# Performance work log

Measured on AMD Instinct MI355X. Metric: run time of the kernel, lower is better.

Reference implementation:

```python
import jax, jax.numpy as jnp
import numpy as np

WIN = 11      # window_size in pytorch_msssim
SIGMA = 1.5   # gaussian sigma in create_window
LEVELS = 5


def _gauss_window(channels, dtype):
    # 1D gaussian -> normalized 2D window, replicated per channel for depthwise conv
    x = jnp.arange(WIN, dtype=dtype) - WIN // 2
    g = jnp.exp(-(x * x) / (2.0 * SIGMA * SIGMA))
    g = g / jnp.sum(g)
    w2 = jnp.outer(g, g)  # [11,11]
    return jnp.broadcast_to(w2[None, None], (channels, 1, WIN, WIN))


def _dwconv(x, w):
    # depthwise valid conv, NCHW (matches F.conv2d(..., padding=0, groups=channel))
    return jax.lax.conv_general_dilated(
        x, w, window_strides=(1, 1), padding='VALID',
        dimension_numbers=('NCHW', 'OIHW', 'NCHW'),
        feature_group_count=x.shape[1])


def _ssim_cs(p, t, w):
    # pytorch_msssim.ssim with full=True, val_range L=1 (inputs in [0,1])
    C1 = 0.01 ** 2
    C2 = 0.03 ** 2
    mu1 = _dwconv(p, w)
    mu2 = _dwconv(t, w)
    mu1_sq = mu1 * mu1
    mu2_sq = mu2 * mu2
    mu1_mu2 = mu1 * mu2
    sigma1_sq = _dwconv(p * p, w) - mu1_sq
    sigma2_sq = _dwconv(t * t, w) - mu2_sq
    sigma12 = _dwconv(p * t, w) - mu1_mu2
    v1 = 2.0 * sigma12 + C2
    v2 = sigma1_sq + sigma2_sq + C2
    # per-category means (axis 1 = the 10 categories, batched as channels)
    cs = jnp.mean(v1 / v2, axis=(0, 2, 3))                                   # [C]
    sim = jnp.mean(((2.0 * mu1_mu2 + C1) * v1) / ((mu1_sq + mu2_sq + C1) * v2),
                   axis=(0, 2, 3))                                           # [C]
    return sim, cs


def _avg_pool2(x):
    n, c, h, w = x.shape
    return x.reshape(n, c, h // 2, 2, w // 2, 2).mean(axis=(3, 5))


def setup_inputs() -> dict:
    key = jax.random.key(0)
    k1, k2 = jax.random.split(key)
    y_pred = jax.random.uniform(k1, (10, 1024, 1024), dtype=jnp.float32)
    y_true = jax.random.uniform(k2, (10, 1024, 1024), dtype=jnp.float32)
    return {"y_pred": y_pred, "y_true": y_true}


def reference(y_pred, y_true):
    # MSSLoss.forward: loss = sum over 10 categories of msssim(pred[c], true[c]);
    # return 1 - mean(loss)  (loss is a scalar, so mean is identity).
    # All 10 per-category msssim calls are batched as channels of one depthwise conv.
    dtype = y_pred.dtype
    weights = jnp.array([0.0448, 0.2856, 0.3001, 0.2363, 0.1333], dtype=dtype)
    p = y_pred[None]  # [1,10,H,W]
    t = y_true[None]
    w = _gauss_window(p.shape[1], dtype)
    sims, css = [], []
    for _ in range(LEVELS):
        s, c = _ssim_cs(p, t, w)
        sims.append(s)
        css.append(c)
        p = _avg_pool2(p)
        t = _avg_pool2(t)
    mssim = jnp.stack(sims)  # [5, 10]
    mcs = jnp.stack(css)     # [5, 10]
    pow1 = mcs ** weights[:, None]
    pow2 = mssim ** weights[:, None]
    # Po-Hsun-Su pytorch_msssim: output = torch.prod(pow1[:-1] * pow2[-1])
    per_cat = jnp.prod(pow1[:-1] * pow2[-1][None, :], axis=0)  # [10]
    return 1.0 - jnp.sum(per_cat)
```

## Files before the change

kernel.cpp:

```cpp
#include <hip/hip_runtime.h>
#include <cstddef>

#define WIN 11
#define HALO 10
#define NCH 10

typedef float v4f __attribute__((ext_vector_type(4)));

constexpr float Gc[WIN] = {
    0.00102838f, 0.00759876f, 0.03600077f, 0.10936069f, 0.21300554f,
    0.26601173f, 0.21300554f, 0.10936069f, 0.03600077f, 0.00759876f,
    0.00102838f};

constexpr int HPITCH = 33;
constexpr int RS = 76;
constexpr int RSZ = RS * HPITCH;

struct Ptrs {
    const float* p[5];
    const float* t[5];
};

__global__ __launch_bounds__(256) void pool_all(
    const float* __restrict__ P0, const float* __restrict__ T0,
    float* __restrict__ p1, float* __restrict__ t1,
    float* __restrict__ p2, float* __restrict__ t2,
    float* __restrict__ p3, float* __restrict__ t3,
    float* __restrict__ p4, float* __restrict__ t4,
    float* __restrict__ acc) {
    __shared__ float sp2[256], st2[256], sp3[64], st3[64];
    const int tid = threadIdx.x;
    if (blockIdx.x == 0 && tid < 128) acc[tid] = 0.f;

    const int b = blockIdx.x;
    const int bx = b & 15, by = (b >> 4) & 15, ch = b >> 8;
    const int tx = tid & 15, ty = tid >> 4;

    const size_t rbase =
        ((size_t)ch * 1024 + by * 64 + ty * 4) * 1024 + bx * 64 + tx * 4;
    float4 pr[4], tr[4];
#pragma unroll
    for (int r2 = 0; r2 < 4; ++r2) {
        pr[r2] = *(const float4*)(P0 + rbase + (size_t)r2 * 1024);
        tr[r2] = *(const float4*)(T0 + rbase + (size_t)r2 * 1024);
    }
    float p1a = 0.25f * ((pr[0].x + pr[0].y) + (pr[1].x + pr[1].y));
    float p1b = 0.25f * ((pr[0].z + pr[0].w) + (pr[1].z + pr[1].w));
    float p1c = 0.25f * ((pr[2].x + pr[2].y) + (pr[3].x + pr[3].y));
    float p1d = 0.25f * ((pr[2].z + pr[2].w) + (pr[3].z + pr[3].w));
    float t1a = 0.25f * ((tr[0].x + tr[0].y) + (tr[1].x + tr[1].y));
    float t1b = 0.25f * ((tr[0].z + tr[0].w) + (tr[1].z + tr[1].w));
    float t1c = 0.25f * ((tr[2].x + tr[2].y) + (tr[3].x + tr[3].y));
    float t1d = 0.25f * ((tr[2].z + tr[2].w) + (tr[3].z + tr[3].w));
    size_t o1 = ((size_t)ch * 512 + by * 32 + ty * 2) * 512 + bx * 32 + tx * 2;
    *(float2*)(p1 + o1) = make_float2(p1a, p1b);
    *(float2*)(p1 + o1 + 512) = make_float2(p1c, p1d);
    *(float2*)(t1 + o1) = make_float2(t1a, t1b);
    *(float2*)(t1 + o1 + 512) = make_float2(t1c, t1d);
    float p2v = 0.25f * ((p1a + p1b) + (p1c + p1d));
    float t2v = 0.25f * ((t1a + t1b) + (t1c + t1d));
    size_t o2 = ((size_t)ch * 256 + by * 16 + ty) * 256 + bx * 16 + tx;
    p2[o2] = p2v;
    t2[o2] = t2v;
    sp2[tid] = p2v;
    st2[tid] = t2v;
    __syncthreads();
    if (tid < 64) {
        int x3 = tid & 7, y3 = tid >> 3;
        int i0 = (2 * y3) * 16 + 2 * x3;
        float p3v = 0.25f * ((sp2[i0] + sp2[i0 + 1]) + (sp2[i0 + 16] + sp2[i0 + 17]));
        float t3v = 0.25f * ((st2[i0] + st2[i0 + 1]) + (st2[i0 + 16] + st2[i0 + 17]));
        size_t o3 = ((size_t)ch * 128 + by * 8 + y3) * 128 + bx * 8 + x3;
        p3[o3] = p3v;
        t3[o3] = t3v;
        sp3[tid] = p3v;
        st3[tid] = t3v;
    }
    __syncthreads();
    if (tid < 16) {
        int x4 = tid & 3, y4 = tid >> 2;
        int i0 = (2 * y4) * 8 + 2 * x4;
        float p4v = 0.25f * ((sp3[i0] + sp3[i0 + 1]) + (sp3[i0 + 8] + sp3[i0 + 9]));
        float t4v = 0.25f * ((st3[i0] + st3[i0 + 1]) + (st3[i0 + 8] + st3[i0 + 9]));
        size_t o4 = ((size_t)ch * 64 + by * 4 + y4) * 64 + bx * 4 + x4;
        p4[o4] = p4v;
        t4[o4] = t4v;
    }
}

__global__ __launch_bounds__(256) void ssim_strip(Ptrs ptrs,
                                                  float* __restrict__ acc) {
    __shared__ v4f hq[RSZ];
    __shared__ float red[8];

    const int bxi = blockIdx.x;
    int lvl, base;
    if (bxi < 128)      { lvl = 0; base = 0; }
    else if (bxi < 160) { lvl = 1; base = 128; }
    else if (bxi < 168) { lvl = 2; base = 160; }
    else if (bxi < 172) { lvl = 3; base = 168; }
    else                { lvl = 4; base = 172; }
    const int local = bxi - base;
    const int H = 1024 >> lvl;
    const int Wout = H - HALO;
    const int ncol = 32 >> lvl;
    const int cs = local & (ncol - 1);
    const int rsi = local >> (5 - lvl);
    const int X0 = cs * 32;
    const int strip_y0 = rsi * 256;
    const int strip_rows = min(256, Wout - strip_y0);
    const int rows_needed = strip_rows + HALO;
    const int nIter = (strip_rows + 31) >> 5;

    const int c = blockIdx.y;
    const float* Pc = ptrs.p[lvl] + (size_t)c * H * H;
    const float* Tc = ptrs.t[lvl] + (size_t)c * H * H;
    const int tid = threadIdx.x;
    const int r6 = tid / 6;
    const int seg = tid - r6 * 6;
    const int x0s = seg * 6;
    const int gxb = X0 + x0s;

    auto load_row = [&](int gy, float2 lp[8], float2 lt[8]) {
        const float* Pr = Pc + (size_t)gy * H + gxb;
        const float* Tr = Tc + (size_t)gy * H + gxb;
        if (gxb + 16 <= H) {
#pragma unroll
            for (int j = 0; j < 8; ++j) {
                lp[j] = *(const float2*)(Pr + 2 * j);
                lt[j] = *(const float2*)(Tr + 2 * j);
            }
        } else {
#pragma unroll
            for (int j = 0; j < 8; ++j) {
                float2 a = make_float2(0.f, 0.f), b = make_float2(0.f, 0.f);
                if (gxb + 2 * j < H)     { a.x = Pr[2 * j];     b.x = Tr[2 * j]; }
                if (gxb + 2 * j + 1 < H) { a.y = Pr[2 * j + 1]; b.y = Tr[2 * j + 1]; }
                lp[j] = a;
                lt[j] = b;
            }
        }
    };

    auto conv_store = [&](int rr, const float2 lp[8], const float2 lt[8]) {
        v4f aq[6] = {};
#pragma unroll
        for (int xi = 0; xi < 16; ++xi) {
            float pv = (xi & 1) ? lp[xi >> 1].y : lp[xi >> 1].x;
            float tv = (xi & 1) ? lt[xi >> 1].y : lt[xi >> 1].x;
            float pp = pv * pv, tt = tv * tv;
            v4f xq = (v4f){pv, tv, pp + tt, pv * tv};
#pragma unroll
            for (int o = 0; o < 6; ++o) {
                int k = xi - o;
                if (k >= 0 && k <= 10) {
                    aq[o] = aq[o] + Gc[k] * xq;
                }
            }
        }
        const int sb = rr * HPITCH;
#pragma unroll
        for (int o = 0; o < 6; ++o) {
            int x = x0s + o;
            if (x < 32) hq[sb + x] = aq[o];
        }
    };

    if (tid < 252) {
        float2 lp[8], lt[8];
        load_row(strip_y0 + r6, lp, lt);
        conv_store(r6, lp, lt);
    }
    __syncthreads();

    float cs_sum = 0.f, sim_sum = 0.f;
    const int txl = tid & 31;
    const int g4 = (tid >> 5) * 4;
    int rrm = r6 + 42;
    if (rrm >= RS) rrm -= RS;
    int y0m = 0;
    for (int i = 0; i < nIter; ++i) {
        float2 lp[8], lt[8];
        const int hrel = 42 + 32 * i + r6;
        const bool doS1 = (tid < 192) && (i + 1 < nIter) && (hrel < rows_needed);
        if (doS1) load_row(strip_y0 + hrel, lp, lt);

        {
            int sl = y0m + g4;
            if (sl >= RS) sl -= RS;
            v4f a[4] = {};
#pragma unroll
            for (int yr = 0; yr < 14; ++yr) {
                v4f vq = hq[sl * HPITCH + txl];
#pragma unroll
                for (int o = 0; o < 4; ++o) {
                    int k = yr - o;
                    if (k >= 0 && k <= 10) {
                        a[o] = a[o] + Gc[k] * vq;
                    }
                }
                ++sl;
                if (sl >= RS) sl = 0;
            }
            const float C1c = 1.0e-4f, C2c = 9.0e-4f;
            const bool colok = (X0 + txl) < Wout;
#pragma unroll
            for (int o = 0; o < 4; ++o) {
                if (colok && (32 * i + g4 + o) < strip_rows) {
                    float mu1 = a[o].x, mu2 = a[o].y;
                    float mu1s = mu1 * mu1, mu2s = mu2 * mu2, mu12 = mu1 * mu2;
                    float v2 = a[o].z - mu1s - mu2s + C2c;
                    float v1 = 2.f * (a[o].w - mu12) + C2c;
                    float den2 = mu1s + mu2s + C1c;
                    float num2 = 2.f * mu12 + C1c;
                    float inv = 1.f / (v2 * den2);
                    cs_sum = fmaf(v1 * den2, inv, cs_sum);
                    sim_sum = fmaf(num2 * v1, inv, sim_sum);
                }
            }
        }

        if (doS1) conv_store(rrm, lp, lt);
        rrm += 32;
        if (rrm >= RS) rrm -= RS;
        y0m += 32;
        if (y0m >= RS) y0m -= RS;
        __syncthreads();
    }

#pragma unroll
    for (int off = 32; off > 0; off >>= 1) {
        cs_sum += __shfl_down(cs_sum, off, 64);
        sim_sum += __shfl_down(sim_sum, off, 64);
    }
    int wave = tid >> 6;
    if ((tid & 63) == 0) {
        red[wave * 2 + 0] = sim_sum;
        red[wave * 2 + 1] = cs_sum;
    }
    __syncthreads();
    if (tid == 0) {
        float s = red[0] + red[2] + red[4] + red[6];
        float cc = red[1] + red[3] + red[5] + red[7];
        atomicAdd(&acc[(lvl * NCH + c) * 2 + 0], s);
        atomicAdd(&acc[(lvl * NCH + c) * 2 + 1], cc);
    }
}

__global__ void finalize_k(const float* __restrict__ acc, float* __restrict__ out) {
    if (threadIdx.x != 0) return;
    const double w[5] = {0.0448, 0.2856, 0.3001, 0.2363, 0.1333};
    const double counts[5] = {1014.0 * 1014.0, 502.0 * 502.0, 246.0 * 246.0,
                              118.0 * 118.0, 54.0 * 54.0};
    double total = 0.0;
    for (int c = 0; c < NCH; ++c) {
        double pc = 1.0;
        for (int l = 0; l < 4; ++l) {
            double mcs = (double)acc[(l * NCH + c) * 2 + 1] / counts[l];
            pc *= pow(mcs, w[l]);
        }
        double ms4 = (double)acc[(4 * NCH + c) * 2 + 0] / counts[4];
        double p2 = pow(ms4, w[4]);
        pc *= (p2 * p2) * (p2 * p2);
        total += pc;
    }
    *out = (float)(1.0 - total);
}

extern "C" void kernel_launch(void* const* d_in, const int* in_sizes, int n_in,
                              void* d_out, int out_size, void* d_ws, size_t ws_size,
                              hipStream_t stream) {
    const float* P0 = (const float*)d_in[0];
    const float* T0 = (const float*)d_in[1];
    float* out = (float*)d_out;
    float* acc = (float*)d_ws;

    const size_t n1 = (size_t)NCH * 512 * 512;
    const size_t n2 = (size_t)NCH * 256 * 256;
    const size_t n3 = (size_t)NCH * 128 * 128;
    const size_t n4 = (size_t)NCH * 64 * 64;
    float* p1 = acc + 128;
    float* t1 = p1 + n1;
    float* p2 = t1 + n1;
    float* t2 = p2 + n2;
    float* p3 = t2 + n2;
    float* t3 = p3 + n3;
    float* p4 = t3 + n3;
    float* t4 = p4 + n4;

    pool_all<<<2560, 256, 0, stream>>>(P0, T0, p1, t1, p2, t2, p3, t3, p4, t4, acc);

    Ptrs ptrs;
    ptrs.p[0] = P0; ptrs.t[0] = T0;
    ptrs.p[1] = p1; ptrs.t[1] = t1;
    ptrs.p[2] = p2; ptrs.t[2] = t2;
    ptrs.p[3] = p3; ptrs.t[3] = t3;
    ptrs.p[4] = p4; ptrs.t[4] = t4;

    ssim_strip<<<dim3(174, NCH, 1), 256, 0, stream>>>(ptrs, acc);

    finalize_k<<<1, 64, 0, stream>>>(acc, out);
}
```

Baseline: 209.7 us.

## Split block into producer and consumer waves for horizontal and vertical conv

The block is split into producer threads (upper half), which register-prefetch the next rows and write horizontal conv results into the shared ring buffer, and consumer threads (lower half), which run the vertical conv plus SSIM math. Each producer now computes 8 outputs from 18 inputs, and each consumer computes 8 output rows from 18 slots, replacing the old 6-wide and 4-row tiles to cut redundant halo work. The goal is to overlap global loads with compute and improve reuse. In exchange only half the threads do the vertical and SSIM math, and register pressure rises, which may lower occupancy.

```diff
diff --git a/kernel.cpp b/kernel.cpp
--- a/kernel.cpp
+++ b/kernel.cpp
@@ -116,23 +116,19 @@
     const float* Pc = ptrs.p[lvl] + (size_t)c * H * H;
     const float* Tc = ptrs.t[lvl] + (size_t)c * H * H;
     const int tid = threadIdx.x;
-    const int r6 = tid / 6;
-    const int seg = tid - r6 * 6;
-    const int x0s = seg * 6;
-    const int gxb = X0 + x0s;
-
-    auto load_row = [&](int gy, float2 lp[8], float2 lt[8]) {
+
+    auto load_row18 = [&](int gy, int gxb, float2 lp[9], float2 lt[9]) {
         const float* Pr = Pc + (size_t)gy * H + gxb;
         const float* Tr = Tc + (size_t)gy * H + gxb;
-        if (gxb + 16 <= H) {
-#pragma unroll
-            for (int j = 0; j < 8; ++j) {
+        if (gxb + 18 <= H) {
+#pragma unroll
+            for (int j = 0; j < 9; ++j) {
                 lp[j] = *(const float2*)(Pr + 2 * j);
                 lt[j] = *(const float2*)(Tr + 2 * j);
             }
         } else {
 #pragma unroll
-            for (int j = 0; j < 8; ++j) {
+            for (int j = 0; j < 9; ++j) {
                 float2 a = make_float2(0.f, 0.f), b = make_float2(0.f, 0.f);
                 if (gxb + 2 * j < H)     { a.x = Pr[2 * j];     b.x = Tr[2 * j]; }
                 if (gxb + 2 * j + 1 < H) { a.y = Pr[2 * j + 1]; b.y = Tr[2 * j + 1]; }
@@ -142,71 +138,79 @@
         }
     };
 
-    auto conv_store = [&](int rr, const float2 lp[8], const float2 lt[8]) {
-        v4f aq[6] = {};
-#pragma unroll
-        for (int xi = 0; xi < 16; ++xi) {
+    auto conv_store8 = [&](int rr, int x0, const float2 lp[9], const float2 lt[9]) {
+        v4f aq[8] = {};
+#pragma unroll
+        for (int xi = 0; xi < 18; ++xi) {
             float pv = (xi & 1) ? lp[xi >> 1].y : lp[xi >> 1].x;
             float tv = (xi & 1) ? lt[xi >> 1].y : lt[xi >> 1].x;
-            float pp = pv * pv, tt = tv * tv;
-            v4f xq = (v4f){pv, tv, pp + tt, pv * tv};
-#pragma unroll
-            for (int o = 0; o < 6; ++o) {
+            v4f xq = (v4f){pv, tv, pv * pv + tv * tv, pv * tv};
+#pragma unroll
+            for (int o = 0; o < 8; ++o) {
                 int k = xi - o;
-                if (k >= 0 && k <= 10) {
-                    aq[o] = aq[o] + Gc[k] * xq;
-                }
-            }
-        }
-        const int sb = rr * HPITCH;
-#pragma unroll
-        for (int o = 0; o < 6; ++o) {
-            int x = x0s + o;
-            if (x < 32) hq[sb + x] = aq[o];
-        }
+                if (k >= 0 && k <= 10) aq[o] = aq[o] + Gc[k] * xq;
+            }
+        }
+        const int sb = rr * HPITCH + x0;
+#pragma unroll
+        for (int o = 0; o < 8; ++o) hq[sb + o] = aq[o];
     };
 
-    if (tid < 252) {
-        float2 lp[8], lt[8];
-        load_row(strip_y0 + r6, lp, lt);
-        conv_store(r6, lp, lt);
+    {
+        const int r = tid >> 2, seg = tid & 3;
+        if (r < 42) {
+            float2 lp[9], lt[9];
+            load_row18(strip_y0 + r, X0 + 8 * seg, lp, lt);
+            conv_store8(r, 8 * seg, lp, lt);
+        }
+    }
+
+    const bool isProd = (tid >= 128);
+    const int pr = tid & 31;
+    const int pseg = (tid >> 5) & 3;
+    float2 plp[9], plt[9];
+    int prRow = 42 + pr;
+    int prSlot = prRow;
+    bool pHave = false;
+    if (isProd && prRow < rows_needed && nIter > 1) {
+        load_row18(strip_y0 + prRow, X0 + 8 * pseg, plp, plt);
+        pHave = true;
     }
     __syncthreads();
 
     float cs_sum = 0.f, sim_sum = 0.f;
     const int txl = tid & 31;
-    const int g4 = (tid >> 5) * 4;
-    int rrm = r6 + 42;
-    if (rrm >= RS) rrm -= RS;
+    const int g = (tid >> 5) & 3;
     int y0m = 0;
     for (int i = 0; i < nIter; ++i) {
-        float2 lp[8], lt[8];
-        const int hrel = 42 + 32 * i + r6;
-        const bool doS1 = (tid < 192) && (i + 1 < nIter) && (hrel < rows_needed);
-        if (doS1) load_row(strip_y0 + hrel, lp, lt);
-
-        {
-            int sl = y0m + g4;
+        if (isProd) {
+            if (pHave) conv_store8(prSlot, 8 * pseg, plp, plt);
+            prSlot += 32;
+            if (prSlot >= RS) prSlot -= RS;
+            prRow += 32;
+            pHave = (prRow < rows_needed) && (i + 2 < nIter + 1) && (i + 1 < nIter);
+            if (pHave) load_row18(strip_y0 + prRow, X0 + 8 * pseg, plp, plt);
+        } else {
+            int sl = y0m + 8 * g;
             if (sl >= RS) sl -= RS;
-            v4f a[4] = {};
-#pragma unroll
-            for (int yr = 0; yr < 14; ++yr) {
+            v4f a[8] = {};
+#pragma unroll
+            for (int yr = 0; yr < 18; ++yr) {
                 v4f vq = hq[sl * HPITCH + txl];
 #pragma unroll
-                for (int o = 0; o < 4; ++o) {
+                for (int o = 0; o < 8; ++o) {
                     int k = yr - o;
-                    if (k >= 0 && k <= 10) {
-                        a[o] = a[o] + Gc[k] * vq;
-                    }
+                    if (k >= 0 && k <= 10) a[o] = a[o] + Gc[k] * vq;
                 }
                 ++sl;
                 if (sl >= RS) sl = 0;
             }
             const float C1c = 1.0e-4f, C2c = 9.0e-4f;
             const bool colok = (X0 + txl) < Wout;
-#pragma unroll
-            for (int o = 0; o < 4; ++o) {
-                if (colok && (32 * i + g4 + o) < strip_rows) {
+            const int orow0 = 32 * i + 8 * g;
+#pragma unroll
+            for (int o = 0; o < 8; ++o) {
+                if (colok && (orow0 + o) < strip_rows) {
                     float mu1 = a[o].x, mu2 = a[o].y;
                     float mu1s = mu1 * mu1, mu2s = mu2 * mu2, mu12 = mu1 * mu2;
                     float v2 = a[o].z - mu1s - mu2s + C2c;
@@ -219,10 +223,6 @@
                 }
             }
         }
-
-        if (doS1) conv_store(rrm, lp, lt);
-        rrm += 32;
-        if (rrm >= RS) rrm -= RS;
         y0m += 32;
         if (y0m >= RS) y0m -= RS;
         __syncthreads();
```

After: 200.6 us. 4.4% less time.
